# Performance work log

Hardware: AMD Instinct MI355X
Metric: run time of the kernel (lower is better)

## Reference

```python
import jax, jax.numpy as jnp
import numpy as np

B = 65536
DI = 512   # image_latent_dim
DT = 256   # text_latent_dim
DC = 512   # combined_latent_dim == max(DI, DT), required by the original module


def setup_inputs() -> dict:
    key = jax.random.key(0)
    ks = jax.random.split(key, 10)
    s = 1.0 / np.sqrt(DC)
    u = lambda k, shape: jax.random.uniform(k, shape, jnp.float32, -s, s)
    return {
        "image_z": jax.random.normal(ks[0], (B, DI), jnp.float32),
        "text_z": jax.random.normal(ks[1], (B, DT), jnp.float32),
        "image_masked": jax.random.randint(ks[2], (B,), 0, 2).astype(bool),
        "text_masked": jax.random.randint(ks[3], (B,), 0, 2).astype(bool),
        "W_ih": u(ks[4], (4 * DC, DC)),
        "W_hh": u(ks[5], (4 * DC, DC)),
        "b_ih": u(ks[6], (4 * DC,)),
        "b_hh": u(ks[7], (4 * DC,)),
        "W_fc": u(ks[8], (2 * DC, DC)),
        "b_fc": u(ks[9], (2 * DC,)),
    }


def _lstm_step(h, c, x, W_ih, W_hh, b_ih, b_hh):
    gates = x @ W_ih.T + b_ih + h @ W_hh.T + b_hh  # [B, 4*DC]
    i, f, g, o = jnp.split(gates, 4, axis=-1)  # PyTorch gate order i,f,g,o
    i = jax.nn.sigmoid(i)
    f = jax.nn.sigmoid(f)
    g = jnp.tanh(g)
    o = jax.nn.sigmoid(o)
    c = f * c + i * g
    h = o * jnp.tanh(c)
    return h, c


def reference(image_z, text_z, image_masked, text_masked, W_ih, W_hh, b_ih, b_hh, W_fc, b_fc):
    Bn = image_z.shape[0]
    img_ok = ~image_masked  # sample contributes image step
    txt_ok = ~text_masked   # sample contributes text step
    # pad each latent to DC (right-pad with zeros), vectorized over batch
    img_p = jnp.pad(image_z, ((0, 0), (0, DC - DI)))
    txt_p = jnp.pad(text_z, ((0, 0), (0, DC - DT)))
    zero = jnp.zeros_like(img_p)
    # step0: image if present, else text if present, else zeros (len-1 zero seq)
    step0 = jnp.where(img_ok[:, None], img_p, jnp.where(txt_ok[:, None], txt_p, zero))
    # step1 only exists when both present
    both = img_ok & txt_ok
    step1 = jnp.where(both[:, None], txt_p, zero)
    h0 = jnp.zeros((Bn, DC), image_z.dtype)
    c0 = jnp.zeros((Bn, DC), image_z.dtype)
    h1, c1 = _lstm_step(h0, c0, step0, W_ih, W_hh, b_ih, b_hh)
    h2, _ = _lstm_step(h1, c1, step1, W_ih, W_hh, b_ih, b_hh)
    # pack_padded_sequence semantics: final hidden taken at true length (1 or 2)
    h_final = jnp.where(both[:, None], h2, h1)
    return h_final @ W_fc.T + b_fc  # [B, 2*DC]
```

## Files before the change

kernel.cpp:

```cpp
#include <hip/hip_runtime.h>
#include <hip/hip_bf16.h>
#include <cstdint>
#include <cstddef>

#define BATCH 65536
#define DCDIM 512
#define DIDIM 512
#define DTDIM 256

typedef __attribute__((ext_vector_type(8))) short short8;
typedef __attribute__((ext_vector_type(4))) float floatx4;

constexpr size_t WS_WA   = 0;
constexpr size_t WS_WCAT = WS_WA   + (size_t)1536*512*2;
constexpr size_t WS_WFC  = WS_WCAT + (size_t)2048*768*2;
constexpr size_t WS_BIAS = WS_WFC  + (size_t)1024*512*2;
constexpr size_t WS_CNT  = WS_BIAS + (size_t)2048*4;
constexpr size_t WS_LIST = WS_CNT  + 256;
constexpr size_t WS_H1   = WS_LIST + (size_t)BATCH*4;
constexpr size_t WS_C1   = WS_H1   + (size_t)BATCH*512*2;
constexpr size_t WS_H2   = WS_C1   + (size_t)BATCH*512*2;

__device__ __forceinline__ unsigned short f2b(float x) {
  unsigned int u = __builtin_bit_cast(unsigned int, x);
  u += 0x7FFFu + ((u >> 16) & 1u);
  return (unsigned short)(u >> 16);
}
__device__ __forceinline__ float b2f(unsigned short h) {
  unsigned int u = ((unsigned int)h) << 16;
  return __builtin_bit_cast(float, u);
}
__device__ __forceinline__ float sigm(float x) { return 1.0f / (1.0f + __expf(-x)); }

__device__ __forceinline__ uint4 pack8(float4 a, float4 b) {
  uint4 w;
  w.x = (unsigned)f2b(a.x) | ((unsigned)f2b(a.y) << 16);
  w.y = (unsigned)f2b(a.z) | ((unsigned)f2b(a.w) << 16);
  w.z = (unsigned)f2b(b.x) | ((unsigned)f2b(b.y) << 16);
  w.w = (unsigned)f2b(b.z) | ((unsigned)f2b(b.w) << 16);
  return w;
}

__global__ void prep_kernel(const float* __restrict__ Wih, const float* __restrict__ Whh,
                            const float* __restrict__ bih, const float* __restrict__ bhh,
                            const float* __restrict__ Wfc,
                            unsigned short* __restrict__ wa, unsigned short* __restrict__ wcat,
                            unsigned short* __restrict__ wfc, float* __restrict__ bias0,
                            int* __restrict__ cnt) {
  int idx = blockIdx.x * blockDim.x + threadIdx.x;
  if (idx == 0) *cnt = 0;
  const int nA = 1536 * 512;
  const int nB = 2048 * 768;
  const int nC = 1024 * 512;
  if (idx < nA) {
    int r = idx >> 9, c = idx & 511;
    int sr = (r < 512) ? r : (r + 512);
    wa[idx] = f2b(Wih[(size_t)sr * 512 + c]);
  } else if (idx < nA + nB) {
    int j = idx - nA;
    int r = j / 768, c = j - r * 768;
    float v = (c < 512) ? Whh[(size_t)r * 512 + c] : Wih[(size_t)r * 512 + (c - 512)];
    wcat[j] = f2b(v);
  } else if (idx < nA + nB + nC) {
    int j = idx - nA - nB;
    wfc[j] = f2b(Wfc[j]);
  } else if (idx < nA + nB + nC + 2048) {
    int j = idx - nA - nB - nC;
    bias0[j] = bih[j] + bhh[j];
  }
}

__global__ void prepass_kernel(const int* __restrict__ imask, const int* __restrict__ tmask,
                               int* __restrict__ cnt, int* __restrict__ list) {
  int m = blockIdx.x * blockDim.x + threadIdx.x;
  if (m < BATCH) {
    if (imask[m] == 0 && tmask[m] == 0) {
      int p = atomicAdd(cnt, 1);
      list[p] = m;
    }
  }
}

__global__ __launch_bounds__(256) void phaseA_kernel(
    const float* __restrict__ img, const float* __restrict__ txt,
    const int* __restrict__ imask, const int* __restrict__ tmask,
    const unsigned short* __restrict__ Wa, const float* __restrict__ bias0,
    unsigned short* __restrict__ h1, unsigned short* __restrict__ c1) {
  __shared__ __align__(16) char smem[50688];
  __shared__ int sel[64];
  char* xs = smem;
  char* wsm = smem + 8192;
  float (*Gs)[64][66] = (float (*)[64][66])smem;

  int tid = threadIdx.x;
  int bx = blockIdx.x;
  int my = bx & 1023, jb = bx >> 10;
  int m0 = my * 64, j0 = jb * 64;
  int wave = tid >> 6, lane = tid & 63, lhi = lane >> 4, llo = lane & 15;

  if (tid < 64) {
    int m = m0 + tid;
    sel[tid] = (imask[m] == 0) ? 0 : ((tmask[m] == 0) ? 1 : 2);
  }
  __syncthreads();

  floatx4 acc[4][3];
  floatx4 zz = {0.f, 0.f, 0.f, 0.f};
#pragma unroll
  for (int a = 0; a < 4; ++a)
#pragma unroll
    for (int b = 0; b < 3; ++b) acc[a][b] = zz;

  for (int kc = 0; kc < 8; ++kc) {
#pragma unroll
    for (int i2 = 0; i2 < 2; ++i2) {
      int f = i2 * 256 + tid;
      int r = f >> 3, sw = f & 7, g = sw ^ (r & 7);
      int kk = kc * 64 + g * 8;
      float4 v0 = {0.f, 0.f, 0.f, 0.f}, v1 = {0.f, 0.f, 0.f, 0.f};
      int s = sel[r];
      if (s == 0) {
        const float4* p = (const float4*)(img + (size_t)(m0 + r) * DIDIM + kk);
        v0 = p[0]; v1 = p[1];
      } else if (s == 1 && kk < DTDIM) {
        const float4* p = (const float4*)(txt + (size_t)(m0 + r) * DTDIM + kk);
        v0 = p[0]; v1 = p[1];
      }
      *(uint4*)(xs + r * 128 + sw * 16) = pack8(v0, v1);
    }
#pragma unroll
    for (int i2 = 0; i2 < 6; ++i2) {
      int f = i2 * 256 + tid;
      int rr = f >> 3, sw = f & 7, g = sw ^ (rr & 7);
      int lg = rr >> 6, jj = rr & 63;
      const uint4* src = (const uint4*)(Wa + ((size_t)(lg * 512 + j0 + jj)) * 512 + kc * 64 + g * 8);
      *(uint4*)(wsm + rr * 128 + sw * 16) = *src;
    }
    __syncthreads();
#pragma unroll
    for (int ks = 0; ks < 2; ++ks) {
      short8 afr[4];
#pragma unroll
      for (int ri = 0; ri < 4; ++ri) {
        int row = ri * 16 + llo;
        int sw = (ks * 4 + lhi) ^ (row & 7);
        afr[ri] = *(const short8*)(xs + row * 128 + sw * 16);
      }
#pragma unroll
      for (int s = 0; s < 3; ++s) {
        int u = 3 * wave + s;
        int lg = u >> 2, ci = u & 3;
        int rr = lg * 64 + ci * 16 + llo;
        int sw = (ks * 4 + lhi) ^ (rr & 7);
        short8 bfr = *(const short8*)(wsm + rr * 128 + sw * 16);
#pragma unroll
        for (int ri = 0; ri < 4; ++ri)
          acc[ri][s] = __builtin_amdgcn_mfma_f32_16x16x32_bf16(afr[ri], bfr, acc[ri][s], 0, 0, 0);
      }
    }
    __syncthreads();
  }
#pragma unroll
  for (int s = 0; s < 3; ++s) {
    int u = 3 * wave + s;
    int lg = u >> 2, ci = u & 3;
#pragma unroll
    for (int ri = 0; ri < 4; ++ri)
#pragma unroll
      for (int p = 0; p < 4; ++p)
        Gs[lg][ri * 16 + lhi * 4 + p][ci * 16 + llo] = acc[ri][s][p];
  }
  __syncthreads();
  {
    int m = tid >> 2;
    int jbase = (tid & 3) * 16;
    size_t rowoff = (size_t)(m0 + m) * DCDIM + j0;
#pragma unroll
    for (int q = 0; q < 16; ++q) {
      int jj = jbase + q;
      int j = j0 + jj;
      float iv = Gs[0][m][jj] + bias0[j];
      float gv = Gs[1][m][jj] + bias0[1024 + j];
      float ov = Gs[2][m][jj] + bias0[1536 + j];
      float iS = sigm(iv), gT = tanhf(gv), oS = sigm(ov);
      float cv = iS * gT;
      float hv = oS * tanhf(cv);
      c1[rowoff + jj] = f2b(cv);
      h1[rowoff + jj] = f2b(hv);
    }
  }
}

__global__ __launch_bounds__(256) void phaseB_kernel(
    const float* __restrict__ txt,
    const unsigned short* __restrict__ h1, const unsigned short* __restrict__ c1,
    const unsigned short* __restrict__ Wcat, const float* __restrict__ bias0,
    const int* __restrict__ cnt, const int* __restrict__ list,
    unsigned short* __restrict__ h2) {
  __shared__ __align__(16) char smem[67584];
  __shared__ int rowmap[64];
  __shared__ int validr[64];
  char* xs = smem;
  char* wsm = smem + 8192;
  float (*Gs)[64][66] = (float (*)[64][66])smem;

  int tid = threadIdx.x;
  int bx = blockIdx.x;
  int my = bx & 1023, jb = bx >> 10;
  int n = *cnt;
  int nbk = (n + 63) >> 6;
  if (my >= nbk) return;
  int j0 = jb * 64;
  int wave = tid >> 6, lane = tid & 63, lhi = lane >> 4, llo = lane & 15;

  if (tid < 64) {
    int p = my * 64 + tid;
    int v = (p < n) ? 1 : 0;
    validr[tid] = v;
    rowmap[tid] = list[v ? p : 0];
  }
  __syncthreads();

  floatx4 acc[4][4];
  floatx4 zz = {0.f, 0.f, 0.f, 0.f};
#pragma unroll
  for (int a = 0; a < 4; ++a)
#pragma unroll
    for (int b = 0; b < 4; ++b) acc[a][b] = zz;

  for (int kc = 0; kc < 12; ++kc) {
#pragma unroll
    for (int i2 = 0; i2 < 2; ++i2) {
      int f = i2 * 256 + tid;
      int r = f >> 3, sw = f & 7, g = sw ^ (r & 7);
      int gm = rowmap[r];
      uint4 w;
      if (kc < 8) {
        w = *(const uint4*)(h1 + (size_t)gm * DCDIM + kc * 64 + g * 8);
      } else {
        int kk = (kc - 8) * 64 + g * 8;
        const float4* p = (const float4*)(txt + (size_t)gm * DTDIM + kk);
        w = pack8(p[0], p[1]);
      }
      *(uint4*)(xs + r * 128 + sw * 16) = w;
    }
#pragma unroll
    for (int i2 = 0; i2 < 8; ++i2) {
      int f = i2 * 256 + tid;
      int rr = f >> 3, sw = f & 7, g = sw ^ (rr & 7);
      int gg = rr >> 6, jj = rr & 63;
      const uint4* src = (const uint4*)(Wcat + ((size_t)(gg * 512 + j0 + jj)) * 768 + kc * 64 + g * 8);
      *(uint4*)(wsm + rr * 128 + sw * 16) = *src;
    }
    __syncthreads();
#pragma unroll
    for (int ks = 0; ks < 2; ++ks) {
      short8 afr[4];
#pragma unroll
      for (int ri = 0; ri < 4; ++ri) {
        int row = ri * 16 + llo;
        int sw = (ks * 4 + lhi) ^ (row & 7);
        afr[ri] = *(const short8*)(xs + row * 128 + sw * 16);
      }
#pragma unroll
      for (int ci = 0; ci < 4; ++ci) {
        int rr = wave * 64 + ci * 16 + llo;
        int sw = (ks * 4 + lhi) ^ (rr & 7);
        short8 bfr = *(const short8*)(wsm + rr * 128 + sw * 16);
#pragma unroll
        for (int ri = 0; ri < 4; ++ri)
          acc[ri][ci] = __builtin_amdgcn_mfma_f32_16x16x32_bf16(afr[ri], bfr, acc[ri][ci], 0, 0, 0);
      }
    }
    __syncthreads();
  }
#pragma unroll
  for (int ci = 0; ci < 4; ++ci)
#pragma unroll
    for (int ri = 0; ri < 4; ++ri)
#pragma unroll
      for (int p = 0; p < 4; ++p)
        Gs[wave][ri * 16 + lhi * 4 + p][ci * 16 + llo] = acc[ri][ci][p];
  __syncthreads();
  {
    int m = tid >> 2;
    if (validr[m]) {
      int gm = rowmap[m];
      int jbase = (tid & 3) * 16;
#pragma unroll
      for (int q = 0; q < 16; ++q) {
        int jj = jbase + q;
        int j = j0 + jj;
        float iv = Gs[0][m][jj] + bias0[j];
        float fv = Gs[1][m][jj] + bias0[512 + j];
        float gv = Gs[2][m][jj] + bias0[1024 + j];
        float ov = Gs[3][m][jj] + bias0[1536 + j];
        float iS = sigm(iv), fS = sigm(fv), gT = tanhf(gv), oS = sigm(ov);
        float c1v = b2f(c1[(size_t)gm * DCDIM + j]);
        float c2 = fS * c1v + iS * gT;
        float h2v = oS * tanhf(c2);
        h2[(size_t)gm * DCDIM + j] = f2b(h2v);
      }
    }
  }
}

__global__ __launch_bounds__(256) void phaseC_kernel(
    const int* __restrict__ imask, const int* __restrict__ tmask,
    const unsigned short* __restrict__ h1, const unsigned short* __restrict__ h2,
    const unsigned short* __restrict__ Wfc, const float* __restrict__ bfc,
    float* __restrict__ out) {
  __shared__ __align__(16) char smem[24576];
  __shared__ int both[64];
  char* xs = smem;
  char* wsm = smem + 8192;
  int tid = threadIdx.x;
  int bx = blockIdx.x;
  int my = bx & 1023, nb = bx >> 10;
  int m0 = my * 64, n0 = nb * 128;
  int wave = tid >> 6, lane = tid & 63, lhi = lane >> 4, llo = lane & 15;
  if (tid < 64) {
    int m = m0 + tid;
    both[tid] = (imask[m] == 0 && tmask[m] == 0) ? 1 : 0;
  }
  __syncthreads();

  floatx4 acc[4][2];
  floatx4 zz = {0.f, 0.f, 0.f, 0.f};
#pragma unroll
  for (int a = 0; a < 4; ++a) { acc[a][0] = zz; acc[a][1] = zz; }

  for (int kc = 0; kc < 8; ++kc) {
#pragma unroll
    for (int i2 = 0; i2 < 2; ++i2) {
      int f = i2 * 256 + tid;
      int r = f >> 3, sw = f & 7, g = sw ^ (r & 7);
      const unsigned short* base = both[r] ? h2 : h1;
      uint4 w = *(const uint4*)(base + (size_t)(m0 + r) * DCDIM + kc * 64 + g * 8);
      *(uint4*)(xs + r * 128 + sw * 16) = w;
    }
#pragma unroll
    for (int i2 = 0; i2 < 4; ++i2) {
      int f = i2 * 256 + tid;
      int rr = f >> 3, sw = f & 7, g = sw ^ (rr & 7);
      const uint4* src = (const uint4*)(Wfc + ((size_t)(n0 + rr)) * 512 + kc * 64 + g * 8);
      *(uint4*)(wsm + rr * 128 + sw * 16) = *src;
    }
    __syncthreads();
#pragma unroll
    for (int ks = 0; ks < 2; ++ks) {
      short8 afr[4];
#pragma unroll
      for (int ri = 0; ri < 4; ++ri) {
        int row = ri * 16 + llo;
        int sw = (ks * 4 + lhi) ^ (row & 7);
        afr[ri] = *(const short8*)(xs + row * 128 + sw * 16);
      }
#pragma unroll
      for (int cl = 0; cl < 2; ++cl) {
        int rr = (wave * 2 + cl) * 16 + llo;
        int sw = (ks * 4 + lhi) ^ (rr & 7);
        short8 bfr = *(const short8*)(wsm + rr * 128 + sw * 16);
#pragma unroll
        for (int ri = 0; ri < 4; ++ri)
          acc[ri][cl] = __builtin_amdgcn_mfma_f32_16x16x32_bf16(afr[ri], bfr, acc[ri][cl], 0, 0, 0);
      }
    }
    __syncthreads();
  }
#pragma unroll
  for (int cl = 0; cl < 2; ++cl) {
    int nn = n0 + (wave * 2 + cl) * 16 + llo;
    float bb = bfc[nn];
#pragma unroll
    for (int ri = 0; ri < 4; ++ri)
#pragma unroll
      for (int p = 0; p < 4; ++p) {
        int mm = m0 + ri * 16 + lhi * 4 + p;
        out[(size_t)mm * 1024 + nn] = acc[ri][cl][p] + bb;
      }
  }
}

extern "C" void kernel_launch(void* const* d_in, const int* in_sizes, int n_in,
                              void* d_out, int out_size, void* d_ws, size_t ws_size,
                              hipStream_t stream) {
  const float* img  = (const float*)d_in[0];
  const float* txt  = (const float*)d_in[1];
  const int* imask  = (const int*)d_in[2];
  const int* tmask  = (const int*)d_in[3];
  const float* Wih  = (const float*)d_in[4];
  const float* Whh  = (const float*)d_in[5];
  const float* bih  = (const float*)d_in[6];
  const float* bhh  = (const float*)d_in[7];
  const float* Wfc  = (const float*)d_in[8];
  const float* bfc  = (const float*)d_in[9];
  float* out = (float*)d_out;

  char* ws = (char*)d_ws;
  unsigned short* wa   = (unsigned short*)(ws + WS_WA);
  unsigned short* wcat = (unsigned short*)(ws + WS_WCAT);
  unsigned short* wfc  = (unsigned short*)(ws + WS_WFC);
  float* bias0         = (float*)(ws + WS_BIAS);
  int* cnt             = (int*)(ws + WS_CNT);
  int* list            = (int*)(ws + WS_LIST);
  unsigned short* h1   = (unsigned short*)(ws + WS_H1);
  unsigned short* c1   = (unsigned short*)(ws + WS_C1);
  unsigned short* h2   = (unsigned short*)(ws + WS_H2);

  prep_kernel<<<11272, 256, 0, stream>>>(Wih, Whh, bih, bhh, Wfc, wa, wcat, wfc, bias0, cnt);
  prepass_kernel<<<256, 256, 0, stream>>>(imask, tmask, cnt, list);
  phaseA_kernel<<<8192, 256, 0, stream>>>(img, txt, imask, tmask, wa, bias0, h1, c1);
  phaseB_kernel<<<8192, 256, 0, stream>>>(txt, h1, c1, wcat, bias0, cnt, list, h2);
  phaseC_kernel<<<8192, 256, 0, stream>>>(imask, tmask, h1, h2, wfc, bfc, out);
}
```

Baseline: 950.2 us.

## Use direct global-to-LDS loads, pre-pack step-0 input, vectorize epilogue stores

```diff
diff --git a/kernel.cpp b/kernel.cpp
--- a/kernel.cpp
+++ b/kernel.cpp
@@ -26,6 +26,9 @@
   u += 0x7FFFu + ((u >> 16) & 1u);
   return (unsigned short)(u >> 16);
 }
+__device__ __forceinline__ unsigned pack2(float a, float b) {
+  return (unsigned)f2b(a) | ((unsigned)f2b(b) << 16);
+}
 __device__ __forceinline__ float b2f(unsigned short h) {
   unsigned int u = ((unsigned int)h) << 16;
   return __builtin_bit_cast(float, u);
@@ -34,11 +37,14 @@
 
 __device__ __forceinline__ uint4 pack8(float4 a, float4 b) {
   uint4 w;
-  w.x = (unsigned)f2b(a.x) | ((unsigned)f2b(a.y) << 16);
-  w.y = (unsigned)f2b(a.z) | ((unsigned)f2b(a.w) << 16);
-  w.z = (unsigned)f2b(b.x) | ((unsigned)f2b(b.y) << 16);
-  w.w = (unsigned)f2b(b.z) | ((unsigned)f2b(b.w) << 16);
+  w.x = pack2(a.x, a.y); w.y = pack2(a.z, a.w);
+  w.z = pack2(b.x, b.y); w.w = pack2(b.z, b.w);
   return w;
+}
+
+__device__ __forceinline__ void gload16(const void* g, void* l) {
+  __builtin_amdgcn_global_load_lds((__attribute__((address_space(1))) void*)g,
+                                   (__attribute__((address_space(3))) void*)l, 16, 0, 0);
 }
 
 __global__ void prep_kernel(const float* __restrict__ Wih, const float* __restrict__ Whh,
@@ -70,6 +76,24 @@
   }
 }
 
+__global__ void prep_x0_kernel(const float* __restrict__ img, const float* __restrict__ txt,
+                               const int* __restrict__ imask, const int* __restrict__ tmask,
+                               unsigned short* __restrict__ X0) {
+  int idx = blockIdx.x * blockDim.x + threadIdx.x;
+  int m = idx >> 6, seg = idx & 63;
+  int s = (imask[m] == 0) ? 0 : ((tmask[m] == 0) ? 1 : 2);
+  int kk = seg * 8;
+  float4 v0 = {0.f, 0.f, 0.f, 0.f}, v1 = {0.f, 0.f, 0.f, 0.f};
+  if (s == 0) {
+    const float4* p = (const float4*)(img + (size_t)m * DIDIM + kk);
+    v0 = p[0]; v1 = p[1];
+  } else if (s == 1 && kk < DTDIM) {
+    const float4* p = (const float4*)(txt + (size_t)m * DTDIM + kk);
+    v0 = p[0]; v1 = p[1];
+  }
+  *(uint4*)(X0 + (size_t)m * DCDIM + kk) = pack8(v0, v1);
+}
+
 __global__ void prepass_kernel(const int* __restrict__ imask, const int* __restrict__ tmask,
                                int* __restrict__ cnt, int* __restrict__ list) {
   int m = blockIdx.x * blockDim.x + threadIdx.x;
@@ -82,12 +106,11 @@
 }
 
 __global__ __launch_bounds__(256) void phaseA_kernel(
-    const float* __restrict__ img, const float* __restrict__ txt,
+    const unsigned short* __restrict__ X0,
     const int* __restrict__ imask, const int* __restrict__ tmask,
     const unsigned short* __restrict__ Wa, const float* __restrict__ bias0,
     unsigned short* __restrict__ h1, unsigned short* __restrict__ c1) {
   __shared__ __align__(16) char smem[50688];
-  __shared__ int sel[64];
   char* xs = smem;
   char* wsm = smem + 8192;
   float (*Gs)[64][66] = (float (*)[64][66])smem;
@@ -98,12 +121,6 @@
   int m0 = my * 64, j0 = jb * 64;
   int wave = tid >> 6, lane = tid & 63, lhi = lane >> 4, llo = lane & 15;
 
-  if (tid < 64) {
-    int m = m0 + tid;
-    sel[tid] = (imask[m] == 0) ? 0 : ((tmask[m] == 0) ? 1 : 2);
-  }
-  __syncthreads();
-
   floatx4 acc[4][3];
   floatx4 zz = {0.f, 0.f, 0.f, 0.f};
 #pragma unroll
@@ -113,28 +130,19 @@
 
   for (int kc = 0; kc < 8; ++kc) {
 #pragma unroll
-    for (int i2 = 0; i2 < 2; ++i2) {
-      int f = i2 * 256 + tid;
-      int r = f >> 3, sw = f & 7, g = sw ^ (r & 7);
-      int kk = kc * 64 + g * 8;
-      float4 v0 = {0.f, 0.f, 0.f, 0.f}, v1 = {0.f, 0.f, 0.f, 0.f};
-      int s = sel[r];
-      if (s == 0) {
-        const float4* p = (const float4*)(img + (size_t)(m0 + r) * DIDIM + kk);
-        v0 = p[0]; v1 = p[1];
-      } else if (s == 1 && kk < DTDIM) {
-        const float4* p = (const float4*)(txt + (size_t)(m0 + r) * DTDIM + kk);
-        v0 = p[0]; v1 = p[1];
-      }
-      *(uint4*)(xs + r * 128 + sw * 16) = pack8(v0, v1);
-    }
-#pragma unroll
-    for (int i2 = 0; i2 < 6; ++i2) {
-      int f = i2 * 256 + tid;
-      int rr = f >> 3, sw = f & 7, g = sw ^ (rr & 7);
+    for (int i = 0; i < 2; ++i) {
+      int c = wave * 2 + i;
+      int r = c * 8 + (lane >> 3);
+      int g = (lane & 7) ^ (r & 7);
+      gload16(X0 + (size_t)(m0 + r) * DCDIM + kc * 64 + g * 8, xs + c * 1024);
+    }
+#pragma unroll
+    for (int i = 0; i < 6; ++i) {
+      int c = wave * 6 + i;
+      int rr = c * 8 + (lane >> 3);
+      int g = (lane & 7) ^ (rr & 7);
       int lg = rr >> 6, jj = rr & 63;
-      const uint4* src = (const uint4*)(Wa + ((size_t)(lg * 512 + j0 + jj)) * 512 + kc * 64 + g * 8);
-      *(uint4*)(wsm + rr * 128 + sw * 16) = *src;
+      gload16(Wa + ((size_t)(lg * 512 + j0 + jj)) * 512 + kc * 64 + g * 8, wsm + c * 1024);
     }
     __syncthreads();
 #pragma unroll
@@ -173,20 +181,35 @@
   __syncthreads();
   {
     int m = tid >> 2;
+    int gm = m0 + m;
     int jbase = (tid & 3) * 16;
-    size_t rowoff = (size_t)(m0 + m) * DCDIM + j0;
-#pragma unroll
-    for (int q = 0; q < 16; ++q) {
-      int jj = jbase + q;
-      int j = j0 + jj;
-      float iv = Gs[0][m][jj] + bias0[j];
-      float gv = Gs[1][m][jj] + bias0[1024 + j];
-      float ov = Gs[2][m][jj] + bias0[1536 + j];
-      float iS = sigm(iv), gT = tanhf(gv), oS = sigm(ov);
-      float cv = iS * gT;
-      float hv = oS * tanhf(cv);
-      c1[rowoff + jj] = f2b(cv);
-      h1[rowoff + jj] = f2b(hv);
+    bool both = (imask[gm] == 0) && (tmask[gm] == 0);
+    size_t rowoff = (size_t)gm * DCDIM + j0;
+    unsigned hp[8], cp[8];
+#pragma unroll
+    for (int q = 0; q < 8; ++q) {
+      float hv[2], cv[2];
+#pragma unroll
+      for (int t = 0; t < 2; ++t) {
+        int jj = jbase + 2 * q + t;
+        int j = j0 + jj;
+        float iv = Gs[0][m][jj] + bias0[j];
+        float gv = Gs[1][m][jj] + bias0[1024 + j];
+        float ov = Gs[2][m][jj] + bias0[1536 + j];
+        float iS = sigm(iv), gT = tanhf(gv), oS = sigm(ov);
+        cv[t] = iS * gT;
+        hv[t] = oS * tanhf(cv[t]);
+      }
+      hp[q] = pack2(hv[0], hv[1]);
+      cp[q] = pack2(cv[0], cv[1]);
+    }
+    uint4* hdst = (uint4*)(h1 + rowoff + jbase);
+    hdst[0] = make_uint4(hp[0], hp[1], hp[2], hp[3]);
+    hdst[1] = make_uint4(hp[4], hp[5], hp[6], hp[7]);
+    if (both) {
+      uint4* cdst = (uint4*)(c1 + rowoff + jbase);
+      cdst[0] = make_uint4(cp[0], cp[1], cp[2], cp[3]);
+      cdst[1] = make_uint4(cp[4], cp[5], cp[6], cp[7]);
     }
   }
 }
@@ -229,28 +252,33 @@
     for (int b = 0; b < 4; ++b) acc[a][b] = zz;
 
   for (int kc = 0; kc < 12; ++kc) {
-#pragma unroll
-    for (int i2 = 0; i2 < 2; ++i2) {
-      int f = i2 * 256 + tid;
-      int r = f >> 3, sw = f & 7, g = sw ^ (r & 7);
-      int gm = rowmap[r];
-      uint4 w;
-      if (kc < 8) {
-        w = *(const uint4*)(h1 + (size_t)gm * DCDIM + kc * 64 + g * 8);
-      } else {
+    if (kc < 8) {
+#pragma unroll
+      for (int i = 0; i < 2; ++i) {
+        int c = wave * 2 + i;
+        int r = c * 8 + (lane >> 3);
+        int g = (lane & 7) ^ (r & 7);
+        int gm = rowmap[r];
+        gload16(h1 + (size_t)gm * DCDIM + kc * 64 + g * 8, xs + c * 1024);
+      }
+    } else {
+#pragma unroll
+      for (int i2 = 0; i2 < 2; ++i2) {
+        int f = i2 * 256 + tid;
+        int r = f >> 3, sw = f & 7, g = sw ^ (r & 7);
+        int gm = rowmap[r];
         int kk = (kc - 8) * 64 + g * 8;
         const float4* p = (const float4*)(txt + (size_t)gm * DTDIM + kk);
-        w = pack8(p[0], p[1]);
-      }
-      *(uint4*)(xs + r * 128 + sw * 16) = w;
-    }
-#pragma unroll
-    for (int i2 = 0; i2 < 8; ++i2) {
-      int f = i2 * 256 + tid;
-      int rr = f >> 3, sw = f & 7, g = sw ^ (rr & 7);
+        *(uint4*)(xs + r * 128 + sw * 16) = pack8(p[0], p[1]);
+      }
+    }
+#pragma unroll
+    for (int i = 0; i < 8; ++i) {
+      int c = wave * 8 + i;
+      int rr = c * 8 + (lane >> 3);
+      int g = (lane & 7) ^ (rr & 7);
       int gg = rr >> 6, jj = rr & 63;
-      const uint4* src = (const uint4*)(Wcat + ((size_t)(gg * 512 + j0 + jj)) * 768 + kc * 64 + g * 8);
-      *(uint4*)(wsm + rr * 128 + sw * 16) = *src;
+      gload16(Wcat + ((size_t)(gg * 512 + j0 + jj)) * 768 + kc * 64 + g * 8, wsm + c * 1024);
     }
     __syncthreads();
 #pragma unroll
@@ -287,20 +315,31 @@
     if (validr[m]) {
       int gm = rowmap[m];
       int jbase = (tid & 3) * 16;
-#pragma unroll
-      for (int q = 0; q < 16; ++q) {
-        int jj = jbase + q;
-        int j = j0 + jj;
-        float iv = Gs[0][m][jj] + bias0[j];
-        float fv = Gs[1][m][jj] + bias0[512 + j];
-        float gv = Gs[2][m][jj] + bias0[1024 + j];
-        float ov = Gs[3][m][jj] + bias0[1536 + j];
-        float iS = sigm(iv), fS = sigm(fv), gT = tanhf(gv), oS = sigm(ov);
-        float c1v = b2f(c1[(size_t)gm * DCDIM + j]);
-        float c2 = fS * c1v + iS * gT;
-        float h2v = oS * tanhf(c2);
-        h2[(size_t)gm * DCDIM + j] = f2b(h2v);
-      }
+      const uint4* csrc = (const uint4*)(c1 + (size_t)gm * DCDIM + j0 + jbase);
+      uint4 cq0 = csrc[0], cq1 = csrc[1];
+      unsigned cw[8] = {cq0.x, cq0.y, cq0.z, cq0.w, cq1.x, cq1.y, cq1.z, cq1.w};
+      unsigned hp[8];
+#pragma unroll
+      for (int q = 0; q < 8; ++q) {
+        float hv[2];
+#pragma unroll
+        for (int t = 0; t < 2; ++t) {
+          int jj = jbase + 2 * q + t;
+          int j = j0 + jj;
+          float iv = Gs[0][m][jj] + bias0[j];
+          float fv = Gs[1][m][jj] + bias0[512 + j];
+          float gv = Gs[2][m][jj] + bias0[1024 + j];
+          float ov = Gs[3][m][jj] + bias0[1536 + j];
+          float iS = sigm(iv), fS = sigm(fv), gT = tanhf(gv), oS = sigm(ov);
+          float c1v = b2f((unsigned short)((cw[q] >> (16 * t)) & 0xFFFFu));
+          float c2 = fS * c1v + iS * gT;
+          hv[t] = oS * tanhf(c2);
+        }
+        hp[q] = pack2(hv[0], hv[1]);
+      }
+      uint4* hdst = (uint4*)(h2 + (size_t)gm * DCDIM + j0 + jbase);
+      hdst[0] = make_uint4(hp[0], hp[1], hp[2], hp[3]);
+      hdst[1] = make_uint4(hp[4], hp[5], hp[6], hp[7]);
     }
   }
 }
@@ -332,19 +371,19 @@
 
   for (int kc = 0; kc < 8; ++kc) {
 #pragma unroll
-    for (int i2 = 0; i2 < 2; ++i2) {
-      int f = i2 * 256 + tid;
-      int r = f >> 3, sw = f & 7, g = sw ^ (r & 7);
+    for (int i = 0; i < 2; ++i) {
+      int c = wave * 2 + i;
+      int r = c * 8 + (lane >> 3);
+      int g = (lane & 7) ^ (r & 7);
       const unsigned short* base = both[r] ? h2 : h1;
-      uint4 w = *(const uint4*)(base + (size_t)(m0 + r) * DCDIM + kc * 64 + g * 8);
-      *(uint4*)(xs + r * 128 + sw * 16) = w;
-    }
-#pragma unroll
-    for (int i2 = 0; i2 < 4; ++i2) {
-      int f = i2 * 256 + tid;
-      int rr = f >> 3, sw = f & 7, g = sw ^ (rr & 7);
-      const uint4* src = (const uint4*)(Wfc + ((size_t)(n0 + rr)) * 512 + kc * 64 + g * 8);
-      *(uint4*)(wsm + rr * 128 + sw * 16) = *src;
+      gload16(base + (size_t)(m0 + r) * DCDIM + kc * 64 + g * 8, xs + c * 1024);
+    }
+#pragma unroll
+    for (int i = 0; i < 4; ++i) {
+      int c = wave * 4 + i;
+      int rr = c * 8 + (lane >> 3);
+      int g = (lane & 7) ^ (rr & 7);
+      gload16(Wfc + ((size_t)(n0 + rr)) * 512 + kc * 64 + g * 8, wsm + c * 1024);
     }
     __syncthreads();
 #pragma unroll
@@ -407,10 +446,12 @@
   unsigned short* h1   = (unsigned short*)(ws + WS_H1);
   unsigned short* c1   = (unsigned short*)(ws + WS_C1);
   unsigned short* h2   = (unsigned short*)(ws + WS_H2);
+  unsigned short* X0   = (unsigned short*)(ws + WS_H2);
 
   prep_kernel<<<11272, 256, 0, stream>>>(Wih, Whh, bih, bhh, Wfc, wa, wcat, wfc, bias0, cnt);
+  prep_x0_kernel<<<16384, 256, 0, stream>>>(img, txt, imask, tmask, X0);
   prepass_kernel<<<256, 256, 0, stream>>>(imask, tmask, cnt, list);
-  phaseA_kernel<<<8192, 256, 0, stream>>>(img, txt, imask, tmask, wa, bias0, h1, c1);
+  phaseA_kernel<<<8192, 256, 0, stream>>>(X0, imask, tmask, wa, bias0, h1, c1);
   phaseB_kernel<<<8192, 256, 0, stream>>>(txt, h1, c1, wcat, bias0, cnt, list, h2);
   phaseC_kernel<<<8192, 256, 0, stream>>>(imask, tmask, h1, h2, wfc, bfc, out);
 }
```

Measured after the change: 913.6 us. 3.9% less time.
